# Kernel optimization log

Measured on AMD Instinct MI355X. Metric: run time of the kernel, lower is better.

The kernel has to match this reference:

```python
import jax, jax.numpy as jnp
import numpy as np

D = 1024   # hidden_dim
F = 4096   # ffn_dim
E = 8      # expert_num
K = 2      # top_k
B, S = 2, 2048

def setup_inputs() -> dict:
    key = jax.random.key(0)
    ks = jax.random.split(key, 5)
    scale = 0.02
    x = jax.random.normal(ks[0], (B, S, D), dtype=jnp.float32)
    gate_w = jax.random.normal(ks[1], (D, E), dtype=jnp.float32) * scale
    w1 = jax.random.normal(ks[2], (E, D, F), dtype=jnp.float32) * scale
    w3 = jax.random.normal(ks[3], (E, D, F), dtype=jnp.float32) * scale
    w2 = jax.random.normal(ks[4], (E, F, D), dtype=jnp.float32) * scale
    return {"x": x, "gate_w": gate_w, "w1": w1, "w3": w3, "w2": w2}

def reference(x, gate_w, w1, w3, w2):
    # x: [B, S, D] -> tokens [T, D]
    Bb, Ss, Dd = x.shape
    xt = x.reshape(-1, Dd)                                  # [T, D]
    T = xt.shape[0]
    # Router: softmax over experts in float32 (matches torch dtype=torch.float)
    router_probs = jax.nn.softmax((xt @ gate_w).astype(jnp.float32), axis=-1)  # [T, E]
    topk_w, topk_idx = jax.lax.top_k(router_probs, K)        # [T, K]
    topk_w = topk_w / topk_w.sum(axis=-1, keepdims=True)
    topk_w = topk_w.astype(x.dtype)
    # Combine weights scattered to dense [T, E] (equivalent to per-expert gather/scatter loop)
    combine = jnp.zeros((T, E), dtype=x.dtype).at[jnp.arange(T)[:, None], topk_idx].add(topk_w)
    # SwishFFN per expert: w2(silu(x w1) * (x w3)), no bias
    h = jax.nn.silu(jnp.einsum('td,edf->etf', xt, w1)) * jnp.einsum('td,edf->etf', xt, w3)  # [E, T, F]
    out_e = jnp.einsum('etf,efd->etd', h, w2)                # [E, T, D]
    out = jnp.einsum('etd,te->td', out_e, combine)           # [T, D]
    return out.reshape(Bb, Ss, Dd), router_probs
```

## Files before the change

kernel.cpp:

```cpp
#include <hip/hip_runtime.h>

typedef unsigned short u16;
typedef unsigned int u32;
typedef __attribute__((ext_vector_type(8))) short bf16x8;
typedef __attribute__((ext_vector_type(4))) float f32x4;
typedef __attribute__((ext_vector_type(4))) int i32x4;
typedef __attribute__((ext_vector_type(2))) unsigned int u32x2;


__device__ __forceinline__ u16 f2bf(float f) {
  u32 u = __builtin_bit_cast(u32, f);
  u += 0x7fffu + ((u >> 16) & 1u);
  return (u16)(u >> 16);
}
__device__ __forceinline__ u32 pack2(u16 a, u16 b) { return (u32)a | ((u32)b << 16); }
__device__ __forceinline__ u32 cvt2(float a, float b) { return pack2(f2bf(a), f2bf(b)); }

__device__ __forceinline__ char* lds_swz(void* base, int row, int byteInRow) {
  return (char*)base + (((row << 7) + byteInRow) ^ ((row & 7) << 4));
}

#define GLL16(g, l) __builtin_amdgcn_global_load_lds( \
    (const __attribute__((address_space(1))) void*)(g), \
    (__attribute__((address_space(3))) void*)(l), 16, 0, 0)

__device__ __forceinline__ void wtrans_tile(const float* __restrict__ src, u16* __restrict__ dst,
                                            int R, int C, int c0, int r0, void* lds)
{
  u16 (*t)[72] = (u16 (*)[72])lds;
  const int tid = threadIdx.x;
  const int rr = (tid >> 4) * 4, cc = (tid & 15) * 4;
  f32x4 v[4];
#pragma unroll
  for (int j = 0; j < 4; ++j) v[j] = *(const f32x4*)(src + (size_t)(r0 + rr + j) * C + c0 + cc);
#pragma unroll
  for (int c = 0; c < 4; ++c) {
    u32x2 p;
    p[0] = pack2(f2bf(v[0][c]), f2bf(v[1][c]));
    p[1] = pack2(f2bf(v[2][c]), f2bf(v[3][c]));
    *(u32x2*)&t[cc + c][rr] = p;
  }
  __syncthreads();
  const int c = tid >> 2, rs = (tid & 3) * 16;
  i32x4 a0 = *(const i32x4*)&t[c][rs];
  i32x4 a1 = *(const i32x4*)&t[c][rs + 8];
  u16* dp = dst + (size_t)(c0 + c) * R + r0 + rs;
  *(i32x4*)dp = a0;
  *(i32x4*)(dp + 8) = a1;
}

__global__ __launch_bounds__(256) void rp_k(
    const float* __restrict__ x, const float* __restrict__ gw,
    float* __restrict__ probs, u16* __restrict__ xb,
    float* __restrict__ wa, int* __restrict__ alist, int* __restrict__ cnt,
    const float* __restrict__ w1, const float* __restrict__ w3,
    u16* __restrict__ w1t, u16* __restrict__ w3t)
{
  __shared__ __align__(16) char smem[9216];
  const int bid = blockIdx.x;
  const int tid = threadIdx.x;

  if (bid >= 128) {
    const int b2 = bid - 128;
    const int sel = b2 >> 13;
    const int t0 = b2 & 8191;
    const int e = t0 >> 10;
    const int rem = t0 & 1023;
    const int xt = rem & 63, yt = rem >> 6;
    const float* src = (sel ? w3 : w1) + (size_t)e * 4194304;
    u16* dst = (sel ? w3t : w1t) + (size_t)e * 4194304;
    wtrans_tile(src, dst, 1024, 4096, xt * 64, yt * 64, smem);
    return;
  }

  int* lcnt  = (int*)smem;
  int* gbase = lcnt + 8;
  int* s_e   = gbase + 8;
  int* s_pos = s_e + 64;
  int* s_row = s_pos + 64;
  float* s_wa = (float*)(s_row + 64);

  const int wv = tid >> 6, l = tid & 63;
  const int tb = bid * 32;

  if (tid < 8) lcnt[tid] = 0;
  __syncthreads();

  for (int i = 0; i < 8; ++i) {
    const int t = tb + wv * 8 + i;
    const float* xrow = x + (size_t)t * 1024;
    f32x4 xv[4];
#pragma unroll
    for (int j = 0; j < 4; ++j) xv[j] = *(const f32x4*)(xrow + j * 256 + l * 4);

    u16* xbt = xb + (size_t)t * 1024;
#pragma unroll
    for (int j = 0; j < 4; ++j) {
      u32x2 hb;
      hb[0] = cvt2(xv[j][0], xv[j][1]);
      hb[1] = cvt2(xv[j][2], xv[j][3]);
      *(u32x2*)(xbt + j * 256 + l * 4) = hb;
    }

    float acc[8];
#pragma unroll
    for (int e = 0; e < 8; ++e) acc[e] = 0.f;
#pragma unroll
    for (int j = 0; j < 4; ++j) {
      const float* g = gw + j * 2048 + l * 32;
#pragma unroll
      for (int c = 0; c < 4; ++c)
#pragma unroll
        for (int e = 0; e < 8; ++e) acc[e] = fmaf(xv[j][c], g[c * 8 + e], acc[e]);
    }
#pragma unroll
    for (int e = 0; e < 8; ++e)
      for (int off = 32; off > 0; off >>= 1) acc[e] += __shfl_down(acc[e], off);

    if (l == 0) {
      float p[8]; float mx = -1e30f;
#pragma unroll
      for (int e = 0; e < 8; ++e) { p[e] = acc[e]; mx = fmaxf(mx, p[e]); }
      float s = 0.f;
#pragma unroll
      for (int e = 0; e < 8; ++e) { p[e] = __expf(p[e] - mx); s += p[e]; }
      float inv = 1.f / s;
#pragma unroll
      for (int e = 0; e < 8; ++e) { p[e] *= inv; probs[(size_t)t * 8 + e] = p[e]; }
      int i0 = 0;
#pragma unroll
      for (int e = 1; e < 8; ++e) if (p[e] > p[i0]) i0 = e;
      int i1 = (i0 == 0) ? 1 : 0;
#pragma unroll
      for (int e = 0; e < 8; ++e) if (e != i0 && p[e] > p[i1]) i1 = e;
      float s2 = p[i0] + p[i1];
      int p0 = atomicAdd(&lcnt[i0], 1);
      int p1 = atomicAdd(&lcnt[i1], 1);
      const int si = (wv * 8 + i) * 2;
      s_e[si] = i0;   s_pos[si] = p0;   s_row[si] = t * 2;
      s_e[si+1] = i1; s_pos[si+1] = p1; s_row[si+1] = t * 2 + 1;
      wa[t * 2]     = p[i0] / s2;
      wa[t * 2 + 1] = p[i1] / s2;
      (void)s_wa;
    }
  }
  __syncthreads();
  if (tid < 8) gbase[tid] = atomicAdd(&cnt[tid], lcnt[tid]);
  __syncthreads();
  if (tid < 64) {
    int e = s_e[tid];
    alist[e * 4096 + gbase[e] + s_pos[tid]] = s_row[tid];
  }
}

__global__ __launch_bounds__(256, 2) void gemm1w2_k(
    const u16* __restrict__ xb, const u16* __restrict__ w1t, const u16* __restrict__ w3t,
    const int* __restrict__ alist, const int* __restrict__ cnt, u16* __restrict__ H,
    const float* __restrict__ w2, u16* __restrict__ w2t)
{
  __shared__ __align__(16) char smem[33280];
  const int e = blockIdx.z;
  const int bx = blockIdx.x;

  if (bx >= 64) {
    const float* src = w2 + (size_t)e * 4194304;
    u16* dst = w2t + (size_t)e * 4194304;
    const int slot = (bx - 64) * 32 + blockIdx.y;
#pragma unroll
    for (int j = 0; j < 4; ++j) {
      const int tj = slot * 4 + j;
      const int cx = tj & 15, ry = tj >> 4;
      wtrans_tile(src, dst, 4096, 1024, cx * 64, ry * 64, smem);
      __syncthreads();
    }
    return;
  }

  u16* As = (u16*)smem;
  u16* Bs = (u16*)(smem + 16384);
  int* rowid = (int*)(smem + 32768);

  const int mc = cnt[e];
  const int m0 = blockIdx.y * 128;
  if (m0 >= mc) return;
  const int n0 = bx * 64;
  const int tid = threadIdx.x;

  if (tid < 128) rowid[tid] = (m0 + tid < mc) ? alist[e * 4096 + m0 + tid] : -1;
  __syncthreads();

  const int l = tid & 63, w = tid >> 6;
  const u16* wt = (w >> 1) ? w3t : w1t;
  u16* bbase = Bs + (w >> 1) * 4096;

  const u16* aps[4]; const u16* bps[4];
  u16* ald[4]; u16* bld[4];
#pragma unroll
  for (int q = 0; q < 4; ++q) {
    int ra = 32 * w + 8 * q + (l >> 3);
    int id = rowid[ra];
    aps[q] = xb + (size_t)(id < 0 ? 0 : (id >> 1)) * 1024 + ((l & 7) ^ (ra & 7)) * 8;
    ald[q] = As + (32 * w + 8 * q) * 64;
    int rb = 32 * (w & 1) + 8 * q + (l >> 3);
    bps[q] = wt + (size_t)e * 4194304 + (size_t)(n0 + rb) * 1024 + ((l & 7) ^ (rb & 7)) * 8;
    bld[q] = bbase + (32 * (w & 1) + 8 * q) * 64;
  }

  const int wm = (w >> 1) * 64, wn = (w & 1) * 32;
  const int l15 = l & 15, lg = l >> 4;

  f32x4 acc1[4][2], acc3[4][2];
  const f32x4 zf = {0.f, 0.f, 0.f, 0.f};
#pragma unroll
  for (int mi = 0; mi < 4; ++mi) { acc1[mi][0] = zf; acc1[mi][1] = zf; acc3[mi][0] = zf; acc3[mi][1] = zf; }

  for (int kt = 0; kt < 16; ++kt) {
    const int ko = kt * 64;
#pragma unroll
    for (int q = 0; q < 4; ++q) GLL16(aps[q] + ko, ald[q]);
#pragma unroll
    for (int q = 0; q < 4; ++q) GLL16(bps[q] + ko, bld[q]);
    __syncthreads();
#pragma unroll
    for (int ks = 0; ks < 2; ++ks) {
      const int kb = ks * 64 + lg * 16;
      bf16x8 af[4];
#pragma unroll
      for (int mi = 0; mi < 4; ++mi)
        af[mi] = *(const bf16x8*)lds_swz(As, wm + mi * 16 + l15, kb);
#pragma unroll
      for (int ni = 0; ni < 2; ++ni) {
        bf16x8 b1 = *(const bf16x8*)lds_swz(Bs, wn + ni * 16 + l15, kb);
        bf16x8 b3 = *(const bf16x8*)lds_swz(Bs + 4096, wn + ni * 16 + l15, kb);
#pragma unroll
        for (int mi = 0; mi < 4; ++mi) {
          acc1[mi][ni] = __builtin_amdgcn_mfma_f32_16x16x32_bf16(af[mi], b1, acc1[mi][ni], 0, 0, 0);
          acc3[mi][ni] = __builtin_amdgcn_mfma_f32_16x16x32_bf16(af[mi], b3, acc3[mi][ni], 0, 0, 0);
        }
      }
    }
    __syncthreads();
  }

#pragma unroll
  for (int mi = 0; mi < 4; ++mi) {
    const int rb = wm + mi * 16 + lg * 4;
#pragma unroll
    for (int ni = 0; ni < 2; ++ni) {
      const int col = n0 + wn + ni * 16 + l15;
      f32x4 c1 = acc1[mi][ni], c3 = acc3[mi][ni];
#pragma unroll
      for (int j = 0; j < 4; ++j) {
        int id = rowid[rb + j];
        if (id >= 0) {
          float a = c1[j];
          float h = (a / (1.f + __expf(-a))) * c3[j];
          H[(size_t)id * 4096 + col] = f2bf(h);
        }
      }
    }
  }
}

__global__ __launch_bounds__(256, 2) void gemm2_k(
    const u16* __restrict__ H, const u16* __restrict__ w2t,
    const int* __restrict__ alist, const int* __restrict__ cnt,
    const float* __restrict__ wa, float* __restrict__ out)
{
  const int e = blockIdx.z;
  const int mc = cnt[e];
  const int yy = blockIdx.y;
  const int kq = yy & 3;
  const int m0 = (yy >> 2) * 128;
  if (m0 >= mc) return;
  const int n0 = blockIdx.x * 128;
  const int tid = threadIdx.x;

  __shared__ u16 As[128 * 64];
  __shared__ u16 Bs[128 * 64];
  __shared__ int rowid[128];
  __shared__ float rw[128];

  if (tid < 128) {
    int id = (m0 + tid < mc) ? alist[e * 4096 + m0 + tid] : -1;
    rowid[tid] = id;
    rw[tid] = (id >= 0) ? wa[id] : 0.f;
  }
  __syncthreads();

  const int l = tid & 63, w = tid >> 6;
  const size_t kbase = (size_t)kq * 1024;
  const u16* aps[4]; const u16* bps[4];
  u16* ald[4]; u16* bld[4];
#pragma unroll
  for (int q = 0; q < 4; ++q) {
    int ra = 32 * w + 8 * q + (l >> 3);
    int id = rowid[ra];
    aps[q] = H + (size_t)(id < 0 ? 0 : id) * 4096 + kbase + ((l & 7) ^ (ra & 7)) * 8;
    ald[q] = As + (32 * w + 8 * q) * 64;
    int rb = 32 * w + 8 * q + (l >> 3);
    bps[q] = w2t + (size_t)e * 4194304 + (size_t)(n0 + rb) * 4096 + kbase + ((l & 7) ^ (rb & 7)) * 8;
    bld[q] = Bs + (32 * w + 8 * q) * 64;
  }

  const int wm = (w >> 1) * 64, wn = (w & 1) * 64;
  const int l15 = l & 15, lg = l >> 4;

  f32x4 acc[4][4];
  const f32x4 zf = {0.f, 0.f, 0.f, 0.f};
#pragma unroll
  for (int mi = 0; mi < 4; ++mi)
#pragma unroll
    for (int ni = 0; ni < 4; ++ni) acc[mi][ni] = zf;

  for (int kt = 0; kt < 16; ++kt) {
    const int ko = kt * 64;
#pragma unroll
    for (int q = 0; q < 4; ++q) GLL16(aps[q] + ko, ald[q]);
#pragma unroll
    for (int q = 0; q < 4; ++q) GLL16(bps[q] + ko, bld[q]);
    __syncthreads();
#pragma unroll
    for (int ks = 0; ks < 2; ++ks) {
      const int kb = ks * 64 + lg * 16;
      bf16x8 af[4];
#pragma unroll
      for (int mi = 0; mi < 4; ++mi)
        af[mi] = *(const bf16x8*)lds_swz(As, wm + mi * 16 + l15, kb);
#pragma unroll
      for (int ni = 0; ni < 4; ++ni) {
        bf16x8 bfb = *(const bf16x8*)lds_swz(Bs, wn + ni * 16 + l15, kb);
#pragma unroll
        for (int mi = 0; mi < 4; ++mi)
          acc[mi][ni] = __builtin_amdgcn_mfma_f32_16x16x32_bf16(af[mi], bfb, acc[mi][ni], 0, 0, 0);
      }
    }
    __syncthreads();
  }

#pragma unroll
  for (int mi = 0; mi < 4; ++mi) {
    const int rb = wm + mi * 16 + lg * 4;
#pragma unroll
    for (int ni = 0; ni < 4; ++ni) {
      const int col = n0 + wn + ni * 16 + l15;
      f32x4 c = acc[mi][ni];
#pragma unroll
      for (int j = 0; j < 4; ++j) {
        int rr = rb + j;
        int id = rowid[rr];
        if (id >= 0)
          unsafeAtomicAdd(&out[(size_t)(id >> 1) * 1024 + col], c[j] * rw[rr]);
      }
    }
  }
}

extern "C" void kernel_launch(void* const* d_in, const int* in_sizes, int n_in,
                              void* d_out, int out_size, void* d_ws, size_t ws_size,
                              hipStream_t stream)
{
  (void)in_sizes; (void)n_in; (void)out_size; (void)ws_size;
  const float* x  = (const float*)d_in[0];
  const float* gw = (const float*)d_in[1];
  const float* w1 = (const float*)d_in[2];
  const float* w3 = (const float*)d_in[3];
  const float* w2 = (const float*)d_in[4];
  float* out   = (float*)d_out;
  float* probs = out + (size_t)4096 * 1024;

  const size_t MB = (size_t)1 << 20;
  char* ws = (char*)d_ws;
  u16*   xb    = (u16*)(ws);
  u16*   H     = (u16*)(ws + 8 * MB);
  u16*   w1t   = (u16*)(ws + 72 * MB);
  u16*   w3t   = (u16*)(ws + 136 * MB);
  u16*   w2t   = (u16*)(ws + 200 * MB);
  float* wa    = (float*)(ws + 264 * MB);
  int*   alist = (int*)(ws + 264 * MB + 32768);
  int*   cnt   = (int*)(ws + 264 * MB + 32768 + 131072);

  (void)hipMemsetAsync(cnt, 0, 8 * sizeof(int), stream);
  (void)hipMemsetAsync(out, 0, (size_t)4096 * 1024 * sizeof(float), stream);
  rp_k<<<16512, 256, 0, stream>>>(x, gw, probs, xb, wa, alist, cnt, w1, w3, w1t, w3t);
  gemm1w2_k<<<dim3(72, 32, 8), 256, 0, stream>>>(xb, w1t, w3t, alist, cnt, H, w2, w2t);
  gemm2_k<<<dim3(8, 128, 8), 256, 0, stream>>>(H, w2t, alist, cnt, wa, out);
}
```

Before: 431.9 us.

## Rewrite expert up-projection GEMM with 256x128 tiles and double-buffered LDS pipeline

Replaces the 128x64 gate/up GEMM (256 threads, single buffer) with a 512-thread kernel computing 256-row by 128-column tiles that interleave w1 and w3 columns. Global-to-LDS loads are double-buffered and split into four phases per k-step, each issuing the next stage's loads before a barrier, with setprio raised around the MFMA bursts. The w2 transpose side-work is repacked so each 512-thread block transposes two tiles at a time across experts. The larger tiles improve operand reuse and overlap memory with compute, but use about 128KB LDS per block, which limits occupancy and makes the hand-placed waitcnt/barrier scheme fragile.

Measured after the change: 520.0 us. 1.2x slower.

```diff
diff --git a/kernel.cpp b/kernel.cpp
--- a/kernel.cpp
+++ b/kernel.cpp
@@ -24,11 +24,10 @@
     (const __attribute__((address_space(1))) void*)(g), \
     (__attribute__((address_space(3))) void*)(l), 16, 0, 0)
 
-__device__ __forceinline__ void wtrans_tile(const float* __restrict__ src, u16* __restrict__ dst,
-                                            int R, int C, int c0, int r0, void* lds)
+__device__ __forceinline__ void wtrans_tile2(const float* __restrict__ src, u16* __restrict__ dst,
+                                             int R, int C, int c0, int r0, void* lds, int tid)
 {
   u16 (*t)[72] = (u16 (*)[72])lds;
-  const int tid = threadIdx.x;
   const int rr = (tid >> 4) * 4, cc = (tid & 15) * 4;
   f32x4 v[4];
 #pragma unroll
@@ -69,7 +68,7 @@
     const int xt = rem & 63, yt = rem >> 6;
     const float* src = (sel ? w3 : w1) + (size_t)e * 4194304;
     u16* dst = (sel ? w3t : w1t) + (size_t)e * 4194304;
-    wtrans_tile(src, dst, 1024, 4096, xt * 64, yt * 64, smem);
+    wtrans_tile2(src, dst, 1024, 4096, xt * 64, yt * 64, smem, tid);
     return;
   }
 
@@ -78,7 +77,6 @@
   int* s_e   = gbase + 8;
   int* s_pos = s_e + 64;
   int* s_row = s_pos + 64;
-  float* s_wa = (float*)(s_row + 64);
 
   const int wv = tid >> 6, l = tid & 63;
   const int tb = bid * 32;
@@ -141,7 +139,6 @@
       s_e[si+1] = i1; s_pos[si+1] = p1; s_row[si+1] = t * 2 + 1;
       wa[t * 2]     = p[i0] / s2;
       wa[t * 2 + 1] = p[i1] / s2;
-      (void)s_wa;
     }
   }
   __syncthreads();
@@ -153,113 +150,144 @@
   }
 }
 
-__global__ __launch_bounds__(256, 2) void gemm1w2_k(
+__global__ __launch_bounds__(512, 2) void gemm1p_k(
     const u16* __restrict__ xb, const u16* __restrict__ w1t, const u16* __restrict__ w3t,
     const int* __restrict__ alist, const int* __restrict__ cnt, u16* __restrict__ H,
     const float* __restrict__ w2, u16* __restrict__ w2t)
 {
-  __shared__ __align__(16) char smem[33280];
+  __shared__ u16 As[2][256][64];
+  __shared__ u16 Bs[2][256][64];
+  __shared__ int rowid[256];
+
   const int e = blockIdx.z;
   const int bx = blockIdx.x;
-
-  if (bx >= 64) {
-    const float* src = w2 + (size_t)e * 4194304;
-    u16* dst = w2t + (size_t)e * 4194304;
-    const int slot = (bx - 64) * 32 + blockIdx.y;
+  const int tid = threadIdx.x;
+
+  if (bx >= 32) {
+    const int half = tid >> 8, t2 = tid & 255;
+    char* psm = (char*)&As[0][0][0] + half * 9216;
+    const int slot = (bx - 32) * 128 + blockIdx.y * 8 + e;
 #pragma unroll
     for (int j = 0; j < 4; ++j) {
-      const int tj = slot * 4 + j;
-      const int cx = tj & 15, ry = tj >> 4;
-      wtrans_tile(src, dst, 4096, 1024, cx * 64, ry * 64, smem);
+      const int tj = slot * 8 + j * 2 + half;
+      const int e2 = tj >> 10, idx = tj & 1023;
+      const float* src = w2 + (size_t)e2 * 4194304;
+      u16* dst = w2t + (size_t)e2 * 4194304;
+      wtrans_tile2(src, dst, 4096, 1024, (idx & 15) * 64, (idx >> 4) * 64, psm, t2);
       __syncthreads();
     }
     return;
   }
 
-  u16* As = (u16*)smem;
-  u16* Bs = (u16*)(smem + 16384);
-  int* rowid = (int*)(smem + 32768);
-
   const int mc = cnt[e];
-  const int m0 = blockIdx.y * 128;
+  const int m0 = blockIdx.y * 256;
   if (m0 >= mc) return;
-  const int n0 = bx * 64;
-  const int tid = threadIdx.x;
-
-  if (tid < 128) rowid[tid] = (m0 + tid < mc) ? alist[e * 4096 + m0 + tid] : -1;
-  __syncthreads();
-
-  const int l = tid & 63, w = tid >> 6;
-  const u16* wt = (w >> 1) ? w3t : w1t;
-  u16* bbase = Bs + (w >> 1) * 4096;
-
-  const u16* aps[4]; const u16* bps[4];
-  u16* ald[4]; u16* bld[4];
-#pragma unroll
-  for (int q = 0; q < 4; ++q) {
-    int ra = 32 * w + 8 * q + (l >> 3);
-    int id = rowid[ra];
-    aps[q] = xb + (size_t)(id < 0 ? 0 : (id >> 1)) * 1024 + ((l & 7) ^ (ra & 7)) * 8;
-    ald[q] = As + (32 * w + 8 * q) * 64;
-    int rb = 32 * (w & 1) + 8 * q + (l >> 3);
-    bps[q] = wt + (size_t)e * 4194304 + (size_t)(n0 + rb) * 1024 + ((l & 7) ^ (rb & 7)) * 8;
-    bld[q] = bbase + (32 * (w & 1) + 8 * q) * 64;
-  }
-
-  const int wm = (w >> 1) * 64, wn = (w & 1) * 32;
+  const int f0 = bx * 128;
+
+  if (tid < 256) rowid[tid] = (m0 + tid < mc) ? alist[e * 4096 + m0 + tid] : -1;
+  __syncthreads();
+
+  const int w = tid >> 6, l = tid & 63;
+  const int wr = w >> 2, wc = w & 3;
   const int l15 = l & 15, lg = l >> 4;
 
-  f32x4 acc1[4][2], acc3[4][2];
+  const u16* aptr[2][2]; const u16* bptr[2][2];
+#pragma unroll
+  for (int hh = 0; hh < 2; ++hh)
+#pragma unroll
+    for (int q = 0; q < 2; ++q) {
+      const int r = hh * 128 + w * 8 + (l >> 3) + q * 64;
+      const int id = rowid[r];
+      aptr[hh][q] = xb + (size_t)(id < 0 ? 0 : (id >> 1)) * 1024 + ((l & 7) ^ (r & 7)) * 8;
+      const int g = r >> 4, sub = r & 15;
+      const int mat = (g >> 2) & 1;
+      const int fg = (g & 3) + ((g >> 3) << 2);
+      const int f = f0 + fg * 16 + sub;
+      bptr[hh][q] = (mat ? w3t : w1t) + (size_t)e * 4194304 + (size_t)f * 1024 + ((l & 7) ^ (r & 7)) * 8;
+    }
+
+#define STAGE_A(B_, H_, KT) do { \
+    GLL16(aptr[H_][0] + (KT) * 64, &As[B_][(H_) * 128 + w * 8][0]); \
+    GLL16(aptr[H_][1] + (KT) * 64, &As[B_][(H_) * 128 + w * 8 + 64][0]); \
+  } while (0)
+#define STAGE_B(B_, H_, KT) do { \
+    GLL16(bptr[H_][0] + (KT) * 64, &Bs[B_][(H_) * 128 + w * 8][0]); \
+    GLL16(bptr[H_][1] + (KT) * 64, &Bs[B_][(H_) * 128 + w * 8 + 64][0]); \
+  } while (0)
+
+  f32x4 acc[8][4];
   const f32x4 zf = {0.f, 0.f, 0.f, 0.f};
 #pragma unroll
-  for (int mi = 0; mi < 4; ++mi) { acc1[mi][0] = zf; acc1[mi][1] = zf; acc3[mi][0] = zf; acc3[mi][1] = zf; }
-
-  for (int kt = 0; kt < 16; ++kt) {
-    const int ko = kt * 64;
-#pragma unroll
-    for (int q = 0; q < 4; ++q) GLL16(aps[q] + ko, ald[q]);
-#pragma unroll
-    for (int q = 0; q < 4; ++q) GLL16(bps[q] + ko, bld[q]);
-    __syncthreads();
-#pragma unroll
-    for (int ks = 0; ks < 2; ++ks) {
-      const int kb = ks * 64 + lg * 16;
-      bf16x8 af[4];
-#pragma unroll
-      for (int mi = 0; mi < 4; ++mi)
-        af[mi] = *(const bf16x8*)lds_swz(As, wm + mi * 16 + l15, kb);
-#pragma unroll
-      for (int ni = 0; ni < 2; ++ni) {
-        bf16x8 b1 = *(const bf16x8*)lds_swz(Bs, wn + ni * 16 + l15, kb);
-        bf16x8 b3 = *(const bf16x8*)lds_swz(Bs + 4096, wn + ni * 16 + l15, kb);
-#pragma unroll
-        for (int mi = 0; mi < 4; ++mi) {
-          acc1[mi][ni] = __builtin_amdgcn_mfma_f32_16x16x32_bf16(af[mi], b1, acc1[mi][ni], 0, 0, 0);
-          acc3[mi][ni] = __builtin_amdgcn_mfma_f32_16x16x32_bf16(af[mi], b3, acc3[mi][ni], 0, 0, 0);
+  for (int mi = 0; mi < 8; ++mi)
+#pragma unroll
+    for (int ni = 0; ni < 4; ++ni) acc[mi][ni] = zf;
+
+#define PHASE(MH, NH, STG) do { \
+    void* Ab = (void*)((char*)&As[0][0][0] + b * 32768); \
+    void* Bb = (void*)((char*)&Bs[0][0][0] + b * 32768); \
+    bf16x8 af[4][2], bfr[2][2]; \
+    _Pragma("unroll") \
+    for (int ks = 0; ks < 2; ++ks) { \
+      _Pragma("unroll") \
+      for (int i = 0; i < 4; ++i) \
+        af[i][ks] = *(const bf16x8*)lds_swz(Ab, (((MH) * 4 + i) * 2 + wr) * 16 + l15, ks * 64 + lg * 16); \
+      _Pragma("unroll") \
+      for (int j = 0; j < 2; ++j) \
+        bfr[j][ks] = *(const bf16x8*)lds_swz(Bb, (((NH) * 2 + j) * 4 + wc) * 16 + l15, ks * 64 + lg * 16); \
+    } \
+    STG; \
+    __builtin_amdgcn_s_barrier(); \
+    __builtin_amdgcn_s_setprio(1); \
+    _Pragma("unroll") \
+    for (int ks = 0; ks < 2; ++ks) \
+      _Pragma("unroll") \
+      for (int i = 0; i < 4; ++i) \
+        _Pragma("unroll") \
+        for (int j = 0; j < 2; ++j) \
+          acc[(MH) * 4 + i][(NH) * 2 + j] = __builtin_amdgcn_mfma_f32_16x16x32_bf16( \
+              af[i][ks], bfr[j][ks], acc[(MH) * 4 + i][(NH) * 2 + j], 0, 0, 0); \
+    __builtin_amdgcn_s_setprio(0); \
+  } while (0)
+
+  STAGE_A(0, 0, 0); STAGE_B(0, 0, 0); STAGE_A(0, 1, 0); STAGE_B(0, 1, 0);
+  STAGE_A(1, 0, 1); STAGE_B(1, 0, 1);
+  asm volatile("s_waitcnt vmcnt(4)" ::: "memory");
+  __builtin_amdgcn_s_barrier();
+
+  for (int t = 0; t < 16; ++t) {
+    const int b = t & 1;
+    PHASE(0, 0, if (t + 1 < 16) STAGE_A(b ^ 1, 1, t + 1));
+    __builtin_amdgcn_s_barrier();
+    PHASE(0, 1, if (t + 1 < 16) STAGE_B(b ^ 1, 1, t + 1));
+    __builtin_amdgcn_s_barrier();
+    PHASE(1, 0, if (t + 2 < 16) STAGE_A(b, 0, t + 2));
+    __builtin_amdgcn_s_barrier();
+    PHASE(1, 1, if (t + 2 < 16) STAGE_B(b, 0, t + 2));
+    if (t <= 13) asm volatile("s_waitcnt vmcnt(4)" ::: "memory");
+    else         asm volatile("s_waitcnt vmcnt(0)" ::: "memory");
+    __builtin_amdgcn_s_barrier();
+  }
+
+#pragma unroll
+  for (int mi = 0; mi < 8; ++mi) {
+    const int rbase = (mi * 2 + wr) * 16 + lg * 4;
+#pragma unroll
+    for (int pr = 0; pr < 2; ++pr) {
+      const int f = f0 + (wc + pr * 4) * 16 + l15;
+      f32x4 c1 = acc[mi][pr * 2], c3 = acc[mi][pr * 2 + 1];
+#pragma unroll
+      for (int j = 0; j < 4; ++j) {
+        int id = rowid[rbase + j];
+        if (id >= 0) {
+          float a = c1[j];
+          H[(size_t)id * 4096 + f] = f2bf((a / (1.f + __expf(-a))) * c3[j]);
         }
       }
     }
-    __syncthreads();
-  }
-
-#pragma unroll
-  for (int mi = 0; mi < 4; ++mi) {
-    const int rb = wm + mi * 16 + lg * 4;
-#pragma unroll
-    for (int ni = 0; ni < 2; ++ni) {
-      const int col = n0 + wn + ni * 16 + l15;
-      f32x4 c1 = acc1[mi][ni], c3 = acc3[mi][ni];
-#pragma unroll
-      for (int j = 0; j < 4; ++j) {
-        int id = rowid[rb + j];
-        if (id >= 0) {
-          float a = c1[j];
-          float h = (a / (1.f + __expf(-a))) * c3[j];
-          H[(size_t)id * 4096 + col] = f2bf(h);
-        }
-      }
-    }
-  }
+  }
+#undef PHASE
+#undef STAGE_A
+#undef STAGE_B
 }
 
 __global__ __launch_bounds__(256, 2) void gemm2_k(
@@ -383,6 +411,6 @@
   (void)hipMemsetAsync(cnt, 0, 8 * sizeof(int), stream);
   (void)hipMemsetAsync(out, 0, (size_t)4096 * 1024 * sizeof(float), stream);
   rp_k<<<16512, 256, 0, stream>>>(x, gw, probs, xb, wa, alist, cnt, w1, w3, w1t, w3t);
-  gemm1w2_k<<<dim3(72, 32, 8), 256, 0, stream>>>(xb, w1t, w3t, alist, cnt, H, w2, w2t);
+  gemm1p_k<<<dim3(40, 16, 8), 512, 0, stream>>>(xb, w1t, w3t, alist, cnt, H, w2, w2t);
   gemm2_k<<<dim3(8, 128, 8), 256, 0, stream>>>(H, w2t, alist, cnt, wa, out);
 }
```
